# Optimization experiments

Measured on AMD Instinct MI355X. Metric: run time of the kernel, lower is better.

## Reference

```python
import jax, jax.numpy as jnp
import numpy as np

NB_FEATURES = 128
ACCUMULATION = 4


def iterative_inv(mat, n_iter=6):
    # Newton-Schulz iteration for matrix inverse ('original' init: global max)
    I = jnp.eye(mat.shape[-1], dtype=mat.dtype)
    K = mat
    V = (1.0 / jnp.max(jnp.sum(K, axis=-2))) * jnp.swapaxes(K, -1, -2)
    for _ in range(n_iter):
        KV = K @ V
        V = 0.25 * V @ (13.0 * I - KV @ (15.0 * I - KV @ (7.0 * I - KV)))
    return V


def setup_inputs() -> dict:
    key = jax.random.key(0)
    kq, kk, kv, ks = jax.random.split(key, 4)
    b, h, n, d = 4, 8, 2048, 64
    q = jax.random.normal(kq, (b, h, n, d), dtype=jnp.float32)
    k = jax.random.normal(kk, (b, h, n, d), dtype=jnp.float32)
    v = jax.random.normal(kv, (b, h, n, d), dtype=jnp.float32)
    mask = jnp.ones((b, n), dtype=jnp.float32)
    total = ACCUMULATION * NB_FEATURES
    # uniform_sketching: indices in [0,n) scaled by non_padding_num (=n here),
    # second half of the flat index list offset by +n to index the k-block of X.
    S = jax.random.randint(ks, (b, total), 0, n)
    S = S.at[:, total // 2:].add(n)
    sketching_matrix = S.reshape(b, ACCUMULATION, NB_FEATURES)
    random_sign = jnp.ones((b, ACCUMULATION, NB_FEATURES), dtype=jnp.float32)
    return {"q": q, "k": k, "v": v, "mask": mask,
            "random_sign": random_sign, "sketching_matrix": sketching_matrix}


def reference(q, k, v, mask, random_sign, sketching_matrix):
    b, h, n, d = q.shape
    data_normalizer = 32.0 ** (-0.25)
    m = mask[:, None, :, None]                      # [b,1,n,1]
    q = q * (m * data_normalizer)
    k = k * (m * data_normalizer)
    v = v * m

    X = jnp.concatenate([q, k], axis=2)             # [b,h,2n,d]
    Xt = jnp.transpose(X, (0, 2, 1, 3))             # [b,2n,h,d]
    XS = Xt[jnp.arange(b)[:, None, None], sketching_matrix]  # [b,acc,f,h,d]
    XS = jnp.transpose(XS, (0, 3, 1, 2, 4))         # [b,h,acc,f,d]

    # RS-RBF kernel sketch: exp(x.y - |x|^2/2 - |y|^2/2), accumulated over acc
    diag1 = (0.5 * jnp.sum(X * X, axis=-1))[:, :, None, :, None]   # [b,h,1,2n,1]
    diag2 = (0.5 * jnp.sum(XS * XS, axis=-1))[:, :, :, None, :]    # [b,h,acc,1,f]
    prod = jnp.einsum('bhnp,bhmfp->bhmnf', X, XS) - diag1 - diag2  # [b,h,acc,2n,f]
    res = jnp.exp(prod)
    res = jnp.transpose(res, (0, 1, 3, 2, 4))       # [b,h,2n,acc,f]
    AS = jnp.einsum('bhnmf,bmf->bhnf', res, random_sign)  # [b,h,2n,f]

    Q = AS[:, :, :n]                                # [b,h,n,f]
    K = AS[:, :, n:]                                # [b,h,n,f]

    ASt = jnp.transpose(AS, (0, 2, 1, 3))           # [b,2n,h,f]
    STAS = ASt[jnp.arange(b)[:, None, None], sketching_matrix]     # [b,acc,f,h,f]
    STAS = jnp.einsum('bmdhe,bmd->bhde', STAS, random_sign)        # [b,h,f,f]
    f = STAS.shape[-1]
    STAS = STAS + 0.1 * jnp.eye(f, dtype=STAS.dtype)

    D_inv = jnp.sqrt(1.0 / jnp.sum(STAS, axis=-1))  # [b,h,f]
    STAS_n = D_inv[..., :, None] * STAS * D_inv[..., None, :]
    STAS_inv = iterative_inv(STAS_n, 6)

    K = (K * D_inv[:, :, None, :]) @ STAS_inv       # [b,h,n,f]
    K = K * D_inv[:, :, None, :] * m

    context = jnp.einsum('bhnf,bhne->bhfe', K, v)   # [b,h,f,d]
    out = Q @ context                               # [b,h,n,d]
    return out
```

## Files before the change

kernel.cpp:

```cpp
#include <hip/hip_runtime.h>

constexpr int Bc = 4, Hc = 8, Nc = 2048, Dc = 64, Fc = 128, Mc = 4;
constexpr int BHc = Bc*Hc;
constexpr int T2c = 2*Nc;
constexpr int Jc  = Mc*Fc;
constexpr float DNORM = 0.4204482076268573f;

constexpr size_t OFF_AS    = 0;
constexpr size_t OFF_XSH   = OFF_AS    + (size_t)BHc*T2c*Fc;
constexpr size_t OFF_XSM   = OFF_XSH   + (size_t)BHc*Jc*Dc/2;
constexpr size_t OFF_XSL   = OFF_XSM   + (size_t)BHc*Jc*Dc/2;
constexpr size_t OFF_DIAG1 = OFF_XSL   + (size_t)BHc*Jc*Dc/2;
constexpr size_t OFF_DIAG2 = OFF_DIAG1 + (size_t)BHc*T2c;
constexpr size_t OFF_STASN = OFF_DIAG2 + (size_t)BHc*Jc;
constexpr size_t OFF_VBUF  = OFF_STASN + (size_t)BHc*Fc*Fc;
constexpr size_t OFF_DINV  = OFF_VBUF  + (size_t)BHc*Fc*Fc;
constexpr size_t OFF_GMAX  = OFF_DINV  + (size_t)BHc*Fc;
constexpr size_t OFF_CTX   = OFF_GMAX  + 64;
constexpr size_t OFF_KH    = OFF_CTX   + (size_t)BHc*Fc*Dc;
constexpr size_t OFF_KM    = OFF_KH    + (size_t)BHc*Fc*Fc/2;
constexpr size_t OFF_KL    = OFF_KM    + (size_t)BHc*Fc*Fc/2;
constexpr size_t OFF_GPART = OFF_XSH;
constexpr size_t OFF_ZSC   = OFF_GPART + (size_t)BHc*4*128*64;

typedef __attribute__((ext_vector_type(8))) short bf16x8;
typedef __attribute__((ext_vector_type(4))) float f32x4;
typedef __attribute__((ext_vector_type(4))) unsigned short u16x4;

__device__ __forceinline__ unsigned short f2bf_rne(float x) {
  unsigned int u = __float_as_uint(x);
  u += 0x7fff + ((u >> 16) & 1);
  return (unsigned short)(u >> 16);
}
__device__ __forceinline__ float bf2f(unsigned short h) {
  return __uint_as_float(((unsigned int)h) << 16);
}

__global__ __launch_bounds__(256) void diag1_kernel(
    const float* __restrict__ q, const float* __restrict__ k,
    const float* __restrict__ mask, float* __restrict__ diag1) {
  int gid = blockIdx.x*256 + threadIdx.x;
  int kq  = gid & 15;
  int row = gid >> 4;
  int t   = row & (T2c - 1);
  int bh  = row >> 12;
  int b   = bh >> 3;
  int tn  = (t < Nc) ? t : t - Nc;
  const float* src = ((t < Nc) ? q : k) + ((size_t)bh*Nc + tn)*Dc;
  float sc = DNORM * mask[b*Nc + tn];
  float4 x = *(const float4*)(src + kq*4);
  float s = x.x*x.x + x.y*x.y + x.z*x.z + x.w*x.w;
  s += __shfl_xor(s, 1);
  s += __shfl_xor(s, 2);
  s += __shfl_xor(s, 4);
  s += __shfl_xor(s, 8);
  if (kq == 0) diag1[row] = 0.5f * sc * sc * s;
}

__global__ __launch_bounds__(256) void gather_kernel(
    const float* __restrict__ q, const float* __restrict__ k,
    const float* __restrict__ mask, const int* __restrict__ sketch,
    const float* __restrict__ diag1,
    unsigned short* __restrict__ xsh, unsigned short* __restrict__ xsm,
    unsigned short* __restrict__ xsl, float* __restrict__ diag2) {
  int gid = blockIdx.x*256 + threadIdx.x;
  int kq  = gid & 15;
  int idx = gid >> 4;
  int j   = idx & (Jc - 1);
  int bh  = idx >> 9;
  int b   = bh >> 3;
  int t   = sketch[b*Jc + j];
  int tn  = (t < Nc) ? t : t - Nc;
  const float* src = ((t < Nc) ? q : k) + ((size_t)bh*Nc + tn)*Dc;
  float sc = DNORM * mask[b*Nc + tn];
  float4 x = *(const float4*)(src + kq*4);
  float xv[4] = {x.x*sc, x.y*sc, x.z*sc, x.w*sc};
  u16x4 hh, mm_, ll;
  #pragma unroll
  for (int jj = 0; jj < 4; ++jj) {
    unsigned short h = f2bf_rne(xv[jj]);
    float r1 = xv[jj] - bf2f(h);
    unsigned short m = f2bf_rne(r1);
    float r2 = r1 - bf2f(m);
    hh[jj] = h; mm_[jj] = m; ll[jj] = f2bf_rne(r2);
  }
  *(u16x4*)(xsh + (size_t)idx*Dc + kq*4) = hh;
  *(u16x4*)(xsm + (size_t)idx*Dc + kq*4) = mm_;
  *(u16x4*)(xsl + (size_t)idx*Dc + kq*4) = ll;
  if (kq == 0) diag2[idx] = diag1[bh*T2c + t];
}

__device__ __forceinline__ unsigned poff(int r, int ke) {
  unsigned byte = ((unsigned)r << 7) | ((unsigned)ke << 1);
  return byte ^ (((unsigned)(r & 7)) << 4);
}

__global__ __launch_bounds__(512) void as_mfma_kernel(
    const float* __restrict__ q, const float* __restrict__ k,
    const float* __restrict__ mask,
    const unsigned short* __restrict__ xsh, const unsigned short* __restrict__ xsm,
    const unsigned short* __restrict__ xsl,
    const float* __restrict__ diag1, const float* __restrict__ diag2,
    const float* __restrict__ sign, float* __restrict__ AS) {
  extern __shared__ char sma[];
  char* Ah = sma;
  char* Am = sma + 16384;
  char* Al = sma + 32768;
  char* Bh = sma + 49152;
  char* Bm = sma + 65536;
  char* Bl = sma + 81920;
  float* d1s = (float*)(sma + 98304);
  float* d2s = (float*)(sma + 98816);
  float* sgs = (float*)(sma + 100864);
  int bh = blockIdx.y, b = bh >> 3;
  int t0 = blockIdx.x * 128;
  int tid = threadIdx.x;
  int lane = tid & 63, wid = tid >> 6;
  int wr = wid >> 1, wc = wid & 1;
  int l16 = lane & 15, lg = lane >> 4;
  int R0 = wr*32, C0 = wc*64;

  for (int i = tid; i < 128*16; i += 512) {
    int r = i >> 4, kq = i & 15;
    int t = t0 + r;
    int tn = (t < Nc) ? t : t - Nc;
    const float* src = ((t < Nc) ? q : k) + ((size_t)bh*Nc + tn)*Dc + kq*4;
    float sc = DNORM * mask[b*Nc + tn];
    float4 x = *(const float4*)src;
    float xv[4] = {x.x*sc, x.y*sc, x.z*sc, x.w*sc};
    u16x4 hv, mv, lv;
    #pragma unroll
    for (int jj = 0; jj < 4; ++jj) {
      unsigned short h = f2bf_rne(xv[jj]);
      float r1 = xv[jj] - bf2f(h);
      unsigned short m = f2bf_rne(r1);
      float r2 = r1 - bf2f(m);
      hv[jj] = h; mv[jj] = m; lv[jj] = f2bf_rne(r2);
    }
    unsigned off = poff(r, kq*4);
    *(u16x4*)(Ah + off) = hv;
    *(u16x4*)(Am + off) = mv;
    *(u16x4*)(Al + off) = lv;
  }
  if (tid < 128) d1s[tid] = diag1[bh*T2c + t0 + tid];
  for (int i = tid; i < 512; i += 512) {
    d2s[i] = diag2[bh*Jc + i];
    sgs[i] = sign[b*Jc + i];
  }

  const unsigned short* xhh = xsh + (size_t)bh*Jc*Dc;
  const unsigned short* xmm = xsm + (size_t)bh*Jc*Dc;
  const unsigned short* xll = xsl + (size_t)bh*Jc*Dc;
  f32x4 oa[2][4];
  #pragma unroll
  for (int m = 0; m < 2; ++m)
    #pragma unroll
    for (int n = 0; n < 4; ++n) oa[m][n] = 0.f;

  for (int m = 0; m < Mc; ++m) {
    __syncthreads();
    for (int i = tid; i < 128*16; i += 512) {
      int c = i >> 4, k4 = i & 15;
      size_t p = (size_t)(m*Fc + c)*Dc + k4*4;
      unsigned off = poff(c, k4*4);
      *(u16x4*)(Bh + off) = *(const u16x4*)(xhh + p);
      *(u16x4*)(Bm + off) = *(const u16x4*)(xmm + p);
      *(u16x4*)(Bl + off) = *(const u16x4*)(xll + p);
    }
    __syncthreads();

    f32x4 acc[2][4];
    #pragma unroll
    for (int mm = 0; mm < 2; ++mm)
      #pragma unroll
      for (int nn = 0; nn < 4; ++nn) acc[mm][nn] = 0.f;
    #pragma unroll
    for (int kc = 0; kc < Dc; kc += 32) {
      int ko = kc + lg*8;
      bf16x8 ah[2], am2[2], al2[2], bhv[4], bmv[4], blv[4];
      #pragma unroll
      for (int mm = 0; mm < 2; ++mm) {
        unsigned off = poff(R0+16*mm+l16, ko);
        ah[mm]  = *(const bf16x8*)(Ah + off);
        am2[mm] = *(const bf16x8*)(Am + off);
        al2[mm] = *(const bf16x8*)(Al + off);
      }
      #pragma unroll
      for (int nn = 0; nn < 4; ++nn) {
        unsigned off = poff(C0+16*nn+l16, ko);
        bhv[nn] = *(const bf16x8*)(Bh + off);
        bmv[nn] = *(const bf16x8*)(Bm + off);
        blv[nn] = *(const bf16x8*)(Bl + off);
      }
      #pragma unroll
      for (int mm = 0; mm < 2; ++mm)
        #pragma unroll
        for (int nn = 0; nn < 4; ++nn) {
          acc[mm][nn] = __builtin_amdgcn_mfma_f32_16x16x32_bf16(am2[mm], bmv[nn], acc[mm][nn], 0,0,0);
          acc[mm][nn] = __builtin_amdgcn_mfma_f32_16x16x32_bf16(ah[mm],  blv[nn], acc[mm][nn], 0,0,0);
          acc[mm][nn] = __builtin_amdgcn_mfma_f32_16x16x32_bf16(al2[mm], bhv[nn], acc[mm][nn], 0,0,0);
          acc[mm][nn] = __builtin_amdgcn_mfma_f32_16x16x32_bf16(ah[mm],  bmv[nn], acc[mm][nn], 0,0,0);
          acc[mm][nn] = __builtin_amdgcn_mfma_f32_16x16x32_bf16(am2[mm], bhv[nn], acc[mm][nn], 0,0,0);
          acc[mm][nn] = __builtin_amdgcn_mfma_f32_16x16x32_bf16(ah[mm],  bhv[nn], acc[mm][nn], 0,0,0);
        }
    }
    #pragma unroll
    for (int mm = 0; mm < 2; ++mm)
      #pragma unroll
      for (int nn = 0; nn < 4; ++nn) {
        int c = C0 + 16*nn + l16;
        float d2v = d2s[m*Fc + c], sg = sgs[m*Fc + c];
        #pragma unroll
        for (int r = 0; r < 4; ++r) {
          int row = R0 + 16*mm + 4*lg + r;
          oa[mm][nn][r] += sg * __expf(acc[mm][nn][r] - d1s[row] - d2v);
        }
      }
  }
  #pragma unroll
  for (int mm = 0; mm < 2; ++mm)
    #pragma unroll
    for (int nn = 0; nn < 4; ++nn) {
      int c = C0 + 16*nn + l16;
      #pragma unroll
      for (int r = 0; r < 4; ++r) {
        int row = R0 + 16*mm + 4*lg + r;
        AS[((size_t)bh*T2c + t0 + row)*Fc + c] = oa[mm][nn][r];
      }
    }
}

__global__ __launch_bounds__(256) void stas_kernel(
    const float* __restrict__ AS, const int* __restrict__ sketch,
    const float* __restrict__ sign,
    float* __restrict__ STASn, float* __restrict__ Dinv,
    unsigned short* __restrict__ Kh, unsigned short* __restrict__ Km,
    unsigned short* __restrict__ Kl,
    unsigned int* __restrict__ gmax) {
  extern __shared__ float stas[];
  __shared__ int   Ssh[Jc];
  __shared__ float sgn[Jc];
  __shared__ float Dl[Fc];
  __shared__ float red[Fc];
  int bh = blockIdx.x;
  int b  = bh >> 3;
  int tid = threadIdx.x;
  for (int i = tid; i < Jc; i += 256) {
    Ssh[i] = sketch[b*Jc + i];
    sgn[i] = sign[b*Jc + i];
  }
  __syncthreads();
  for (int i = tid; i < Fc*Fc; i += 256) {
    int dd = i >> 7, e = i & 127;
    float vsum = 0.f;
    #pragma unroll
    for (int m = 0; m < Mc; ++m) {
      int t = Ssh[m*Fc + dd];
      vsum += sgn[m*Fc + dd] * AS[((size_t)bh*T2c + t)*Fc + e];
    }
    if (dd == e) vsum += 0.1f;
    stas[dd*129 + e] = vsum;
  }
  __syncthreads();
  if (tid < Fc) {
    float s = 0.f;
    for (int e = 0; e < Fc; ++e) s += stas[tid*129 + e];
    float di = 1.0f / sqrtf(s);
    Dl[tid] = di;
    Dinv[bh*Fc + tid] = di;
  }
  __syncthreads();
  for (int i = tid; i < Fc*Fc; i += 256) {
    int dd = i >> 7, e = i & 127;
    float vv = stas[dd*129 + e] * Dl[dd] * Dl[e];
    stas[dd*129 + e] = vv;
    STASn[(size_t)bh*Fc*Fc + i] = vv;
    unsigned short hb = f2bf_rne(vv); float r1 = vv - bf2f(hb);
    unsigned short mb = f2bf_rne(r1); float r2 = r1 - bf2f(mb);
    Kh[(size_t)bh*Fc*Fc + i] = hb;
    Km[(size_t)bh*Fc*Fc + i] = mb;
    Kl[(size_t)bh*Fc*Fc + i] = f2bf_rne(r2);
  }
  __syncthreads();
  if (tid < Fc) {
    float s = 0.f;
    for (int dd = 0; dd < Fc; ++dd) s += stas[dd*129 + tid];
    red[tid] = s;
  }
  __syncthreads();
  if (tid == 0) {
    float mx = 0.f;
    for (int e = 0; e < Fc; ++e) mx = fmaxf(mx, red[e]);
    atomicMax(gmax, __float_as_uint(mx));
  }
}

__device__ __forceinline__ unsigned boff(int brow, int ke) {
  unsigned byte = ((unsigned)brow << 8) | ((unsigned)ke << 1);
  return byte ^ (((unsigned)(brow & 7)) << 4);
}

__device__ __forceinline__ void mm6(const bf16x8 ah[2], const bf16x8 am[2], const bf16x8 al[2],
                                    const bf16x8 bh[4], const bf16x8 bm[4], const bf16x8 bl[4],
                                    f32x4 acc[2][4]) {
  #pragma unroll
  for (int m = 0; m < 2; ++m)
    #pragma unroll
    for (int n = 0; n < 4; ++n) {
      acc[m][n] = __builtin_amdgcn_mfma_f32_16x16x32_bf16(am[m], bm[n], acc[m][n], 0,0,0);
      acc[m][n] = __builtin_amdgcn_mfma_f32_16x16x32_bf16(ah[m], bl[n], acc[m][n], 0,0,0);
      acc[m][n] = __builtin_amdgcn_mfma_f32_16x16x32_bf16(al[m], bh[n], acc[m][n], 0,0,0);
      acc[m][n] = __builtin_amdgcn_mfma_f32_16x16x32_bf16(ah[m], bm[n], acc[m][n], 0,0,0);
      acc[m][n] = __builtin_amdgcn_mfma_f32_16x16x32_bf16(am[m], bh[n], acc[m][n], 0,0,0);
      acc[m][n] = __builtin_amdgcn_mfma_f32_16x16x32_bf16(ah[m], bh[n], acc[m][n], 0,0,0);
    }
}

__device__ __forceinline__ void ld3(const char* Ph, const char* Pm, const char* Pl,
                                    int brow, int ko, bf16x8& h, bf16x8& m, bf16x8& l) {
  unsigned off = boff(brow, ko);
  h = *(const bf16x8*)(Ph + off);
  m = *(const bf16x8*)(Pm + off);
  l = *(const bf16x8*)(Pl + off);
}

__device__ __forceinline__ void mm_p1(
    const unsigned short* __restrict__ kh, const unsigned short* __restrict__ km,
    const unsigned short* __restrict__ kl,
    const char* Ah, const char* Am, const char* Al,
    int R0, int C0, int l16, int lg, f32x4 acc[2][4]) {
  #pragma unroll 2
  for (int kc = 0; kc < Fc; kc += 32) {
    int ko = kc + lg*8;
    bf16x8 ah[2], am[2], al[2], bh[4], bm[4], bl[4];
    #pragma unroll
    for (int m = 0; m < 2; ++m) {
      size_t p = (size_t)(R0+16*m+l16)*Fc + ko;
      ah[m] = *(const bf16x8*)(kh + p);
      am[m] = *(const bf16x8*)(km + p);
      al[m] = *(const bf16x8*)(kl + p);
    }
    #pragma unroll
    for (int n = 0; n < 4; ++n)
      ld3(Ah, Am, Al, C0+16*n+l16, ko, bh[n], bm[n], bl[n]);
    mm6(ah, am, al, bh, bm, bl, acc);
  }
}

__device__ __forceinline__ void mm_p234(
    const char* Ah, const char* Am, const char* Al,
    const char* Zh, const char* Zm, const unsigned short* __restrict__ ZlG,
    int R0, int C0, int l16, int lg, f32x4 acc[2][4]) {
  #pragma unroll 1
  for (int kc = 0; kc < Fc; kc += 32) {
    int ko = kc + lg*8;
    bf16x8 ah[2], am[2], al[2], bh[4], bm[4], bl[4];
    #pragma unroll
    for (int m = 0; m < 2; ++m)
      ld3(Ah, Am, Al, R0+16*m+l16, ko, ah[m], am[m], al[m]);
    #pragma unroll
    for (int n = 0; n < 4; ++n) {
      int col = C0+16*n+l16;
      unsigned off = boff(col, ko);
      bh[n] = *(const bf16x8*)(Zh + off);
      bm[n] = *(const bf16x8*)(Zm + off);
      bl[n] = *(const bf16x8*)(ZlG + col*Fc + ko);
    }
    mm6(ah, am, al, bh, bm, bl, acc);
  }
}

__device__ __forceinline__ void split4(f32x4 v, u16x4& hv, u16x4& mv, u16x4& lv) {
  #pragma unroll
  for (int r = 0; r < 4; ++r) {
    unsigned short hb = f2bf_rne(v[r]); float r1 = v[r] - bf2f(hb);
    unsigned short mb = f2bf_rne(r1);   float r2 = r1 - bf2f(mb);
    hv[r] = hb; mv[r] = mb; lv[r] = f2bf_rne(r2);
  }
}
__device__ __forceinline__ void wbA3(char* Ah, char* Am, char* Al,
                                     int col, int row0, f32x4 v) {
  u16x4 hv, mv, lv;
  split4(v, hv, mv, lv);
  unsigned off = boff(col, row0);
  *(u16x4*)(Ah + off) = hv;
  *(u16x4*)(Am + off) = mv;
  *(u16x4*)(Al + off) = lv;
}
__device__ __forceinline__ void wbZ3(char* Zh, char* Zm, unsigned short* __restrict__ ZlG,
                                     int col, int row0, f32x4 v) {
  u16x4 hv, mv, lv;
  split4(v, hv, mv, lv);
  unsigned off = boff(col, row0);
  *(u16x4*)(Zh + off) = hv;
  *(u16x4*)(Zm + off) = mv;
  *(u16x4*)(ZlG + col*Fc + row0) = lv;
}

__global__ __launch_bounds__(512) void newton_ctx_kernel(
    const float* __restrict__ STASn,
    const unsigned short* __restrict__ KhG, const unsigned short* __restrict__ KmG,
    const unsigned short* __restrict__ KlG,
    const float* __restrict__ gmaxf, float* __restrict__ Vout,
    const float* __restrict__ ASg, const float* __restrict__ vg,
    const float* __restrict__ maskg, float* __restrict__ Gpart,
    unsigned short* __restrict__ ZlScr) {
  extern __shared__ char smc[];
  int tid  = threadIdx.x;

  if (blockIdx.x < BHc) {
    char* Ah = smc;
    char* Am = smc + 32768;
    char* Al = smc + 65536;
    char* Zh = smc + 98304;
    char* Zm = smc + 131072;
    int bh = blockIdx.x;
    const float* Kp = STASn + (size_t)bh*Fc*Fc;
    const unsigned short* kh = KhG + (size_t)bh*Fc*Fc;
    const unsigned short* km = KmG + (size_t)bh*Fc*Fc;
    const unsigned short* kl = KlG + (size_t)bh*Fc*Fc;
    unsigned short* ZlG = ZlScr + (size_t)bh*Fc*Fc;
    float ginv = 1.0f / gmaxf[0];
    int lane = tid & 63;
    int wid  = tid >> 6;
    int wr = wid >> 1, wc = wid & 1;
    int l16 = lane & 15, lg = lane >> 4;
    int R0 = wr*32, C0 = wc*64;
    int drow0 = lg*4;

    f32x4 vreg[2][4];
    #pragma unroll
    for (int m = 0; m < 2; ++m)
      #pragma unroll
      for (int n = 0; n < 4; ++n) {
        int col = C0 + 16*n + l16;
        #pragma unroll
        for (int r = 0; r < 4; ++r)
          vreg[m][n][r] = Kp[(size_t)(R0 + 16*m + drow0 + r)*Fc + col] * ginv;
        wbA3(Ah, Am, Al, col, R0 + 16*m + drow0, vreg[m][n]);
      }
    __syncthreads();

    f32x4 fin[2][4];
    for (int it = 0; it < 6; ++it) {
      f32x4 acc[2][4];
      #pragma unroll
      for (int m = 0; m < 2; ++m) for (int n = 0; n < 4; ++n) acc[m][n] = 0.f;
      mm_p1(kh, km, kl, Ah, Am, Al, R0, C0, l16, lg, acc);
      #pragma unroll
      for (int m = 0; m < 2; ++m)
        #pragma unroll
        for (int n = 0; n < 4; ++n)
          wbZ3(Zh, Zm, ZlG, C0 + 16*n + l16, R0 + 16*m + drow0, acc[m][n]);
      __syncthreads();

      #pragma unroll
      for (int m = 0; m < 2; ++m) for (int n = 0; n < 4; ++n) acc[m][n] = 0.f;
      mm_p234(Ah, Am, Al, Zh, Zm, ZlG, R0, C0, l16, lg, acc);
      #pragma unroll
      for (int m = 0; m < 2; ++m)
        #pragma unroll
        for (int n = 0; n < 4; ++n)
          fin[m][n] = 13.f*vreg[m][n] - 15.f*acc[m][n];
      __syncthreads();
      #pragma unroll
      for (int m = 0; m < 2; ++m)
        #pragma unroll
        for (int n = 0; n < 4; ++n)
          wbA3(Ah, Am, Al, C0 + 16*n + l16, R0 + 16*m + drow0, acc[m][n]);
      __syncthreads();

      #pragma unroll
      for (int m = 0; m < 2; ++m) for (int n = 0; n < 4; ++n) acc[m][n] = 0.f;
      mm_p234(Ah, Am, Al, Zh, Zm, ZlG, R0, C0, l16, lg, acc);
      #pragma unroll
      for (int m = 0; m < 2; ++m)
        #pragma unroll
        for (int n = 0; n < 4; ++n)
          fin[m][n] += 7.f*acc[m][n];
      __syncthreads();
      #pragma unroll
      for (int m = 0; m < 2; ++m)
        #pragma unroll
        for (int n = 0; n < 4; ++n)
          wbA3(Ah, Am, Al, C0 + 16*n + l16, R0 + 16*m + drow0, acc[m][n]);
      __syncthreads();

      #pragma unroll
      for (int m = 0; m < 2; ++m) for (int n = 0; n < 4; ++n) acc[m][n] = 0.f;
      mm_p234(Ah, Am, Al, Zh, Zm, ZlG, R0, C0, l16, lg, acc);
      #pragma unroll
      for (int m = 0; m < 2; ++m)
        #pragma unroll
        for (int n = 0; n < 4; ++n) {
          fin[m][n] = 0.25f*(fin[m][n] - acc[m][n]);
          vreg[m][n] = fin[m][n];
        }
      __syncthreads();
      #pragma unroll
      for (int m = 0; m < 2; ++m)
        #pragma unroll
        for (int n = 0; n < 4; ++n)
          wbA3(Ah, Am, Al, C0 + 16*n + l16, R0 + 16*m + drow0, fin[m][n]);
      __syncthreads();
    }

    float* Vo = Vout + (size_t)bh*Fc*Fc;
    #pragma unroll
    for (int m = 0; m < 2; ++m)
      #pragma unroll
      for (int n = 0; n < 4; ++n) {
        int col = C0 + 16*n + l16;
        #pragma unroll
        for (int r = 0; r < 4; ++r)
          Vo[(size_t)(R0 + 16*m + drow0 + r)*Fc + col] = vreg[m][n][r];
      }
  } else {
    float* Ksh = (float*)smc;
    float* vsh = (float*)(smc + 32768);
    int id = blockIdx.x - BHc;
    int cbh = id >> 2, chunk = id & 3;
    int cb = cbh >> 3;
    int t0 = chunk * 512;
    int f = tid & 127, g = tid >> 7;
    float acc[16];
    #pragma unroll
    for (int j = 0; j < 16; ++j) acc[j] = 0.f;
    for (int sub = 0; sub < 8; ++sub) {
      __syncthreads();
      int ts = t0 + sub*64;
      for (int i = tid; i < 64*32; i += 512) {
        int r = i >> 5, c4 = i & 31;
        *(float4*)&Ksh[r*128 + c4*4] =
            *(const float4*)(ASg + ((size_t)cbh*T2c + Nc + ts + r)*Fc + c4*4);
      }
      for (int i = tid; i < 64*16; i += 512) {
        int r = i >> 4, c4 = i & 15;
        float mk = maskg[cb*Nc + ts + r];
        float m2 = mk*mk;
        float4 x = *(const float4*)(vg + ((size_t)cbh*Nc + ts + r)*Dc + c4*4);
        x.x*=m2; x.y*=m2; x.z*=m2; x.w*=m2;
        *(float4*)&vsh[r*64 + c4*4] = x;
      }
      __syncthreads();
      #pragma unroll 2
      for (int tl = 0; tl < 64; ++tl) {
        float kf = Ksh[tl*128 + f];
        #pragma unroll
        for (int j4 = 0; j4 < 4; ++j4) {
          float4 vv = *(const float4*)&vsh[tl*64 + g*16 + j4*4];
          acc[j4*4+0] += kf*vv.x; acc[j4*4+1] += kf*vv.y;
          acc[j4*4+2] += kf*vv.z; acc[j4*4+3] += kf*vv.w;
        }
      }
    }
    float* gp = Gpart + ((((size_t)cbh*4 + chunk)*128 + f)*64 + g*16);
    #pragma unroll
    for (int j4 = 0; j4 < 4; ++j4)
      *(float4*)(gp + j4*4) = *(const float4*)&acc[j4*4];
  }
}

__global__ __launch_bounds__(256) void ctx_fix_kernel(
    const float* __restrict__ Gpart, const float* __restrict__ Vinv,
    const float* __restrict__ Dinv, float* __restrict__ ctxo) {
  __shared__ float DG[128*64];
  __shared__ float Dl[128];
  int bh = blockIdx.x;
  int tid = threadIdx.x;
  if (tid < 128) Dl[tid] = Dinv[bh*Fc + tid];
  __syncthreads();
  for (int i = tid; i < 2048; i += 256) {
    int e = i >> 4, c4 = i & 15;
    const float* g0 = Gpart + ((((size_t)bh*4)*128 + e)*64 + c4*4);
    float4 s0 = *(const float4*)(g0);
    float4 s1 = *(const float4*)(g0 + 8192);
    float4 s2 = *(const float4*)(g0 + 16384);
    float4 s3 = *(const float4*)(g0 + 24576);
    float de = Dl[e];
    float4 o;
    o.x = (s0.x+s1.x+s2.x+s3.x)*de;
    o.y = (s0.y+s1.y+s2.y+s3.y)*de;
    o.z = (s0.z+s1.z+s2.z+s3.z)*de;
    o.w = (s0.w+s1.w+s2.w+s3.w)*de;
    *(float4*)&DG[e*64 + c4*4] = o;
  }
  __syncthreads();
  int f = tid & 127, half = tid >> 7;
  float acc[32];
  #pragma unroll
  for (int j = 0; j < 32; ++j) acc[j] = 0.f;
  for (int e = 0; e < 128; ++e) {
    float s = Vinv[(size_t)bh*Fc*Fc + (size_t)e*Fc + f];
    #pragma unroll
    for (int j4 = 0; j4 < 8; ++j4) {
      float4 dg = *(const float4*)&DG[e*64 + half*32 + j4*4];
      acc[j4*4+0] += s*dg.x; acc[j4*4+1] += s*dg.y;
      acc[j4*4+2] += s*dg.z; acc[j4*4+3] += s*dg.w;
    }
  }
  float df = Dl[f];
  float* op = ctxo + (size_t)bh*Fc*Dc + f*Dc + half*32;
  #pragma unroll
  for (int j4 = 0; j4 < 8; ++j4) {
    float4 o;
    o.x = acc[j4*4+0]*df; o.y = acc[j4*4+1]*df;
    o.z = acc[j4*4+2]*df; o.w = acc[j4*4+3]*df;
    *(float4*)(op + j4*4) = o;
  }
}

__global__ __launch_bounds__(256) void out_kernel(
    const float* __restrict__ AS, const float* __restrict__ ctx,
    float* __restrict__ out) {
  extern __shared__ float smo[];
  float* Asq = smo;
  float* Cs  = smo + 64*132;
  int bh = blockIdx.y;
  int row0 = blockIdx.x * 64;
  int tid = threadIdx.x;
  int tr = tid >> 4, tc = tid & 15;
  for (int i = tid; i < 64*32; i += 256) {
    int r = i >> 5, kq = i & 31;
    *(float4*)&Asq[r*132 + kq*4] =
        *(const float4*)(AS + ((size_t)bh*T2c + row0 + r)*Fc + kq*4);
  }
  for (int i = tid; i < 128*16; i += 256) {
    int r = i >> 4, kq = i & 15;
    *(float4*)&Cs[r*64 + kq*4] =
        *(const float4*)(ctx + (size_t)bh*Fc*Dc + r*Dc + kq*4);
  }
  __syncthreads();
  float acc[4][4] = {};
  #pragma unroll 2
  for (int kk = 0; kk < Fc; ++kk) {
    float4 bv = *(const float4*)&Cs[kk*64 + tc*4];
    float a0 = Asq[(tr*4+0)*132 + kk];
    float a1 = Asq[(tr*4+1)*132 + kk];
    float a2 = Asq[(tr*4+2)*132 + kk];
    float a3 = Asq[(tr*4+3)*132 + kk];
    acc[0][0] += a0*bv.x; acc[0][1] += a0*bv.y; acc[0][2] += a0*bv.z; acc[0][3] += a0*bv.w;
    acc[1][0] += a1*bv.x; acc[1][1] += a1*bv.y; acc[1][2] += a1*bv.z; acc[1][3] += a1*bv.w;
    acc[2][0] += a2*bv.x; acc[2][1] += a2*bv.y; acc[2][2] += a2*bv.z; acc[2][3] += a2*bv.w;
    acc[3][0] += a3*bv.x; acc[3][1] += a3*bv.y; acc[3][2] += a3*bv.z; acc[3][3] += a3*bv.w;
  }
  #pragma unroll
  for (int i = 0; i < 4; ++i) {
    float4 o;
    o.x = acc[i][0]; o.y = acc[i][1]; o.z = acc[i][2]; o.w = acc[i][3];
    *(float4*)(out + ((size_t)bh*Nc + row0 + tr*4 + i)*Dc + tc*4) = o;
  }
}

extern "C" void kernel_launch(void* const* d_in, const int* in_sizes, int n_in,
                              void* d_out, int out_size, void* d_ws, size_t ws_size,
                              hipStream_t stream) {
  const float* q    = (const float*)d_in[0];
  const float* k    = (const float*)d_in[1];
  const float* v    = (const float*)d_in[2];
  const float* mask = (const float*)d_in[3];
  const float* sign = (const float*)d_in[4];
  const int*   sketch = (const int*)d_in[5];
  float* out = (float*)d_out;
  float* ws  = (float*)d_ws;

  unsigned short* xsh = (unsigned short*)(ws + OFF_XSH);
  unsigned short* xsm = (unsigned short*)(ws + OFF_XSM);
  unsigned short* xsl = (unsigned short*)(ws + OFF_XSL);
  unsigned short* kh  = (unsigned short*)(ws + OFF_KH);
  unsigned short* km  = (unsigned short*)(ws + OFF_KM);
  unsigned short* kl  = (unsigned short*)(ws + OFF_KL);
  unsigned short* zsc = (unsigned short*)(ws + OFF_ZSC);

  hipMemsetAsync(ws + OFF_GMAX, 0, sizeof(float), stream);

  diag1_kernel<<<BHc*T2c*16/256, 256, 0, stream>>>(q, k, mask, ws + OFF_DIAG1);
  gather_kernel<<<BHc*Jc*16/256, 256, 0, stream>>>(q, k, mask, sketch, ws + OFF_DIAG1,
                                                   xsh, xsm, xsl, ws + OFF_DIAG2);
  as_mfma_kernel<<<dim3(T2c/128, BHc), 512, 102912, stream>>>(q, k, mask, xsh, xsm, xsl,
      ws + OFF_DIAG1, ws + OFF_DIAG2, sign, ws + OFF_AS);
  stas_kernel<<<BHc, 256, 128*129*sizeof(float), stream>>>(ws + OFF_AS, sketch, sign,
      ws + OFF_STASN, ws + OFF_DINV, kh, km, kl, (unsigned int*)(ws + OFF_GMAX));
  newton_ctx_kernel<<<BHc + 128, 512, 163840, stream>>>(ws + OFF_STASN, kh, km, kl,
      ws + OFF_GMAX, ws + OFF_VBUF, ws + OFF_AS, v, mask, ws + OFF_GPART, zsc);
  ctx_fix_kernel<<<BHc, 256, 0, stream>>>(ws + OFF_GPART, ws + OFF_VBUF,
      ws + OFF_DINV, ws + OFF_CTX);
  out_kernel<<<dim3(Nc/64, BHc), 256, (64*132 + 128*64)*sizeof(float), stream>>>(
      ws + OFF_AS, ws + OFF_CTX, out);
}
```

Baseline: 331.6 us.

## Compute sketched AS rows first and overlap full AS with Newton iterations

A new small kernel computes the RBF sketch only for the 512 sketched rows per head. STAS is now built from those rows, so it no longer has to wait for the full AS matrix. The full AS computation moves into the same launch as the serial Newton-Schulz inverse, running on the spare blocks while the 32 Newton blocks work. The context accumulation becomes its own kernel afterwards. In exchange, the sketched rows' exponentials are computed twice (about one eighth extra AS work) and the launch gains an extra kernel. The scratch buffer is moved so it no longer aliases the gather buffers, which are now still being read during the Newton launch.

After: 343.3 us. +3.5%, slower.

```diff
diff --git a/kernel.cpp b/kernel.cpp
--- a/kernel.cpp
+++ b/kernel.cpp
@@ -20,8 +20,9 @@
 constexpr size_t OFF_KH    = OFF_CTX   + (size_t)BHc*Fc*Dc;
 constexpr size_t OFF_KM    = OFF_KH    + (size_t)BHc*Fc*Fc/2;
 constexpr size_t OFF_KL    = OFF_KM    + (size_t)BHc*Fc*Fc/2;
+constexpr size_t OFF_ZSC   = OFF_KL    + (size_t)BHc*Fc*Fc/2;
 constexpr size_t OFF_GPART = OFF_XSH;
-constexpr size_t OFF_ZSC   = OFF_GPART + (size_t)BHc*4*128*64;
+constexpr size_t OFF_ASS   = OFF_AS;
 
 typedef __attribute__((ext_vector_type(8))) short bf16x8;
 typedef __attribute__((ext_vector_type(4))) float f32x4;
@@ -95,14 +96,10 @@
   return byte ^ (((unsigned)(r & 7)) << 4);
 }
 
-__global__ __launch_bounds__(512) void as_mfma_kernel(
-    const float* __restrict__ q, const float* __restrict__ k,
-    const float* __restrict__ mask,
-    const unsigned short* __restrict__ xsh, const unsigned short* __restrict__ xsm,
-    const unsigned short* __restrict__ xsl,
-    const float* __restrict__ diag1, const float* __restrict__ diag2,
-    const float* __restrict__ sign, float* __restrict__ AS) {
-  extern __shared__ char sma[];
+__device__ __forceinline__ void as_body(
+    char* sma, const unsigned short* xhh, const unsigned short* xmm,
+    const unsigned short* xll, float* __restrict__ dst, size_t dst_row_stride_base,
+    int tid) {
   char* Ah = sma;
   char* Am = sma + 16384;
   char* Al = sma + 32768;
@@ -112,45 +109,11 @@
   float* d1s = (float*)(sma + 98304);
   float* d2s = (float*)(sma + 98816);
   float* sgs = (float*)(sma + 100864);
-  int bh = blockIdx.y, b = bh >> 3;
-  int t0 = blockIdx.x * 128;
-  int tid = threadIdx.x;
   int lane = tid & 63, wid = tid >> 6;
   int wr = wid >> 1, wc = wid & 1;
   int l16 = lane & 15, lg = lane >> 4;
   int R0 = wr*32, C0 = wc*64;
 
-  for (int i = tid; i < 128*16; i += 512) {
-    int r = i >> 4, kq = i & 15;
-    int t = t0 + r;
-    int tn = (t < Nc) ? t : t - Nc;
-    const float* src = ((t < Nc) ? q : k) + ((size_t)bh*Nc + tn)*Dc + kq*4;
-    float sc = DNORM * mask[b*Nc + tn];
-    float4 x = *(const float4*)src;
-    float xv[4] = {x.x*sc, x.y*sc, x.z*sc, x.w*sc};
-    u16x4 hv, mv, lv;
-    #pragma unroll
-    for (int jj = 0; jj < 4; ++jj) {
-      unsigned short h = f2bf_rne(xv[jj]);
-      float r1 = xv[jj] - bf2f(h);
-      unsigned short m = f2bf_rne(r1);
-      float r2 = r1 - bf2f(m);
-      hv[jj] = h; mv[jj] = m; lv[jj] = f2bf_rne(r2);
-    }
-    unsigned off = poff(r, kq*4);
-    *(u16x4*)(Ah + off) = hv;
-    *(u16x4*)(Am + off) = mv;
-    *(u16x4*)(Al + off) = lv;
-  }
-  if (tid < 128) d1s[tid] = diag1[bh*T2c + t0 + tid];
-  for (int i = tid; i < 512; i += 512) {
-    d2s[i] = diag2[bh*Jc + i];
-    sgs[i] = sign[b*Jc + i];
-  }
-
-  const unsigned short* xhh = xsh + (size_t)bh*Jc*Dc;
-  const unsigned short* xmm = xsm + (size_t)bh*Jc*Dc;
-  const unsigned short* xll = xsl + (size_t)bh*Jc*Dc;
   f32x4 oa[2][4];
   #pragma unroll
   for (int m = 0; m < 2; ++m)
@@ -225,39 +188,64 @@
       #pragma unroll
       for (int r = 0; r < 4; ++r) {
         int row = R0 + 16*mm + 4*lg + r;
-        AS[((size_t)bh*T2c + t0 + row)*Fc + c] = oa[mm][nn][r];
+        dst[dst_row_stride_base + (size_t)row*Fc + c] = oa[mm][nn][r];
       }
     }
 }
 
+__global__ __launch_bounds__(512) void ass_mfma_kernel(
+    const unsigned short* __restrict__ xsh, const unsigned short* __restrict__ xsm,
+    const unsigned short* __restrict__ xsl,
+    const float* __restrict__ diag2, const float* __restrict__ sign,
+    float* __restrict__ ASS) {
+  extern __shared__ char sma[];
+  float* d1s = (float*)(sma + 98304);
+  float* d2s = (float*)(sma + 98816);
+  float* sgs = (float*)(sma + 100864);
+  int bh = blockIdx.y, b = bh >> 3;
+  int j0 = blockIdx.x * 128;
+  int tid = threadIdx.x;
+  const unsigned short* xhh = xsh + (size_t)bh*Jc*Dc;
+  const unsigned short* xmm = xsm + (size_t)bh*Jc*Dc;
+  const unsigned short* xll = xsl + (size_t)bh*Jc*Dc;
+
+  for (int i = tid; i < 128*16; i += 512) {
+    int r = i >> 4, kq = i & 15;
+    size_t p = (size_t)(j0 + r)*Dc + kq*4;
+    unsigned off = poff(r, kq*4);
+    *(u16x4*)(sma + off)         = *(const u16x4*)(xhh + p);
+    *(u16x4*)(sma + 16384 + off) = *(const u16x4*)(xmm + p);
+    *(u16x4*)(sma + 32768 + off) = *(const u16x4*)(xll + p);
+  }
+  if (tid < 128) d1s[tid] = diag2[bh*Jc + j0 + tid];
+  for (int i = tid; i < 512; i += 512) {
+    d2s[i] = diag2[bh*Jc + i];
+    sgs[i] = sign[b*Jc + i];
+  }
+  as_body(sma, xhh, xmm, xll, ASS, (size_t)bh*Jc*Fc + (size_t)j0*Fc, tid);
+}
+
 __global__ __launch_bounds__(256) void stas_kernel(
-    const float* __restrict__ AS, const int* __restrict__ sketch,
-    const float* __restrict__ sign,
+    const float* __restrict__ ASS, const float* __restrict__ sign,
     float* __restrict__ STASn, float* __restrict__ Dinv,
     unsigned short* __restrict__ Kh, unsigned short* __restrict__ Km,
     unsigned short* __restrict__ Kl,
     unsigned int* __restrict__ gmax) {
   extern __shared__ float stas[];
-  __shared__ int   Ssh[Jc];
   __shared__ float sgn[Jc];
   __shared__ float Dl[Fc];
   __shared__ float red[Fc];
   int bh = blockIdx.x;
   int b  = bh >> 3;
   int tid = threadIdx.x;
-  for (int i = tid; i < Jc; i += 256) {
-    Ssh[i] = sketch[b*Jc + i];
-    sgn[i] = sign[b*Jc + i];
-  }
+  for (int i = tid; i < Jc; i += 256) sgn[i] = sign[b*Jc + i];
   __syncthreads();
   for (int i = tid; i < Fc*Fc; i += 256) {
     int dd = i >> 7, e = i & 127;
     float vsum = 0.f;
     #pragma unroll
-    for (int m = 0; m < Mc; ++m) {
-      int t = Ssh[m*Fc + dd];
-      vsum += sgn[m*Fc + dd] * AS[((size_t)bh*T2c + t)*Fc + e];
-    }
+    for (int m = 0; m < Mc; ++m)
+      vsum += sgn[m*Fc + dd] * ASS[((size_t)bh*Jc + m*Fc + dd)*Fc + e];
     if (dd == e) vsum += 0.1f;
     stas[dd*129 + e] = vsum;
   }
@@ -397,14 +385,18 @@
   *(u16x4*)(ZlG + col*Fc + row0) = lv;
 }
 
-__global__ __launch_bounds__(512) void newton_ctx_kernel(
+__global__ __launch_bounds__(512) void newton_as_kernel(
     const float* __restrict__ STASn,
     const unsigned short* __restrict__ KhG, const unsigned short* __restrict__ KmG,
     const unsigned short* __restrict__ KlG,
     const float* __restrict__ gmaxf, float* __restrict__ Vout,
-    const float* __restrict__ ASg, const float* __restrict__ vg,
-    const float* __restrict__ maskg, float* __restrict__ Gpart,
-    unsigned short* __restrict__ ZlScr) {
+    unsigned short* __restrict__ ZlScr,
+    const float* __restrict__ q, const float* __restrict__ k,
+    const float* __restrict__ mask,
+    const unsigned short* __restrict__ xsh, const unsigned short* __restrict__ xsm,
+    const unsigned short* __restrict__ xsl,
+    const float* __restrict__ diag1, const float* __restrict__ diag2,
+    const float* __restrict__ sign, float* __restrict__ AS) {
   extern __shared__ char smc[];
   int tid  = threadIdx.x;
 
@@ -516,49 +508,94 @@
           Vo[(size_t)(R0 + 16*m + drow0 + r)*Fc + col] = vreg[m][n][r];
       }
   } else {
-    float* Ksh = (float*)smc;
-    float* vsh = (float*)(smc + 32768);
     int id = blockIdx.x - BHc;
-    int cbh = id >> 2, chunk = id & 3;
-    int cb = cbh >> 3;
-    int t0 = chunk * 512;
-    int f = tid & 127, g = tid >> 7;
-    float acc[16];
-    #pragma unroll
-    for (int j = 0; j < 16; ++j) acc[j] = 0.f;
-    for (int sub = 0; sub < 8; ++sub) {
-      __syncthreads();
-      int ts = t0 + sub*64;
-      for (int i = tid; i < 64*32; i += 512) {
-        int r = i >> 5, c4 = i & 31;
-        *(float4*)&Ksh[r*128 + c4*4] =
-            *(const float4*)(ASg + ((size_t)cbh*T2c + Nc + ts + r)*Fc + c4*4);
+    int bh = id >> 5, b = bh >> 3;
+    int t0 = (id & 31) * 128;
+    float* d1s = (float*)(smc + 98304);
+    float* d2s = (float*)(smc + 98816);
+    float* sgs = (float*)(smc + 100864);
+
+    for (int i = tid; i < 128*16; i += 512) {
+      int r = i >> 4, kq = i & 15;
+      int t = t0 + r;
+      int tn = (t < Nc) ? t : t - Nc;
+      const float* src = ((t < Nc) ? q : k) + ((size_t)bh*Nc + tn)*Dc + kq*4;
+      float sc = DNORM * mask[b*Nc + tn];
+      float4 x = *(const float4*)src;
+      float xv[4] = {x.x*sc, x.y*sc, x.z*sc, x.w*sc};
+      u16x4 hv, mv, lv;
+      #pragma unroll
+      for (int jj = 0; jj < 4; ++jj) {
+        unsigned short h = f2bf_rne(xv[jj]);
+        float r1 = xv[jj] - bf2f(h);
+        unsigned short m = f2bf_rne(r1);
+        float r2 = r1 - bf2f(m);
+        hv[jj] = h; mv[jj] = m; lv[jj] = f2bf_rne(r2);
       }
-      for (int i = tid; i < 64*16; i += 512) {
-        int r = i >> 4, c4 = i & 15;
-        float mk = maskg[cb*Nc + ts + r];
-        float m2 = mk*mk;
-        float4 x = *(const float4*)(vg + ((size_t)cbh*Nc + ts + r)*Dc + c4*4);
-        x.x*=m2; x.y*=m2; x.z*=m2; x.w*=m2;
-        *(float4*)&vsh[r*64 + c4*4] = x;
+      unsigned off = poff(r, kq*4);
+      *(u16x4*)(smc + off)         = hv;
+      *(u16x4*)(smc + 16384 + off) = mv;
+      *(u16x4*)(smc + 32768 + off) = lv;
+    }
+    if (tid < 128) d1s[tid] = diag1[bh*T2c + t0 + tid];
+    for (int i = tid; i < 512; i += 512) {
+      d2s[i] = diag2[bh*Jc + i];
+      sgs[i] = sign[b*Jc + i];
+    }
+    const unsigned short* xhh = xsh + (size_t)bh*Jc*Dc;
+    const unsigned short* xmm = xsm + (size_t)bh*Jc*Dc;
+    const unsigned short* xll = xsl + (size_t)bh*Jc*Dc;
+    as_body(smc, xhh, xmm, xll, AS, (size_t)bh*T2c*Fc + (size_t)t0*Fc, tid);
+  }
+}
+
+__global__ __launch_bounds__(512) void ctx_raw_kernel(
+    const float* __restrict__ ASg, const float* __restrict__ vg,
+    const float* __restrict__ maskg, float* __restrict__ Gpart) {
+  extern __shared__ char smc[];
+  float* Ksh = (float*)smc;
+  float* vsh = (float*)(smc + 32768);
+  int id = blockIdx.x;
+  int cbh = id >> 2, chunk = id & 3;
+  int cb = cbh >> 3;
+  int t0 = chunk * 512;
+  int tid = threadIdx.x;
+  int f = tid & 127, g = tid >> 7;
+  float acc[16];
+  #pragma unroll
+  for (int j = 0; j < 16; ++j) acc[j] = 0.f;
+  for (int sub = 0; sub < 8; ++sub) {
+    __syncthreads();
+    int ts = t0 + sub*64;
+    for (int i = tid; i < 64*32; i += 512) {
+      int r = i >> 5, c4 = i & 31;
+      *(float4*)&Ksh[r*128 + c4*4] =
+          *(const float4*)(ASg + ((size_t)cbh*T2c + Nc + ts + r)*Fc + c4*4);
+    }
+    for (int i = tid; i < 64*16; i += 512) {
+      int r = i >> 4, c4 = i & 15;
+      float mk = maskg[cb*Nc + ts + r];
+      float m2 = mk*mk;
+      float4 x = *(const float4*)(vg + ((size_t)cbh*Nc + ts + r)*Dc + c4*4);
+      x.x*=m2; x.y*=m2; x.z*=m2; x.w*=m2;
+      *(float4*)&vsh[r*64 + c4*4] = x;
+    }
+    __syncthreads();
+    #pragma unroll 2
+    for (int tl = 0; tl < 64; ++tl) {
+      float kf = Ksh[tl*128 + f];
+      #pragma unroll
+      for (int j4 = 0; j4 < 4; ++j4) {
+        float4 vv = *(const float4*)&vsh[tl*64 + g*16 + j4*4];
+        acc[j4*4+0] += kf*vv.x; acc[j4*4+1] += kf*vv.y;
+        acc[j4*4+2] += kf*vv.z; acc[j4*4+3] += kf*vv.w;
       }
-      __syncthreads();
-      #pragma unroll 2
-      for (int tl = 0; tl < 64; ++tl) {
-        float kf = Ksh[tl*128 + f];
-        #pragma unroll
-        for (int j4 = 0; j4 < 4; ++j4) {
-          float4 vv = *(const float4*)&vsh[tl*64 + g*16 + j4*4];
-          acc[j4*4+0] += kf*vv.x; acc[j4*4+1] += kf*vv.y;
-          acc[j4*4+2] += kf*vv.z; acc[j4*4+3] += kf*vv.w;
-        }
-      }
-    }
-    float* gp = Gpart + ((((size_t)cbh*4 + chunk)*128 + f)*64 + g*16);
-    #pragma unroll
-    for (int j4 = 0; j4 < 4; ++j4)
-      *(float4*)(gp + j4*4) = *(const float4*)&acc[j4*4];
-  }
+    }
+  }
+  float* gp = Gpart + ((((size_t)cbh*4 + chunk)*128 + f)*64 + g*16);
+  #pragma unroll
+  for (int j4 = 0; j4 < 4; ++j4)
+    *(float4*)(gp + j4*4) = *(const float4*)&acc[j4*4];
 }
 
 __global__ __launch_bounds__(256) void ctx_fix_kernel(
@@ -677,12 +714,14 @@
   diag1_kernel<<<BHc*T2c*16/256, 256, 0, stream>>>(q, k, mask, ws + OFF_DIAG1);
   gather_kernel<<<BHc*Jc*16/256, 256, 0, stream>>>(q, k, mask, sketch, ws + OFF_DIAG1,
                                                    xsh, xsm, xsl, ws + OFF_DIAG2);
-  as_mfma_kernel<<<dim3(T2c/128, BHc), 512, 102912, stream>>>(q, k, mask, xsh, xsm, xsl,
-      ws + OFF_DIAG1, ws + OFF_DIAG2, sign, ws + OFF_AS);
-  stas_kernel<<<BHc, 256, 128*129*sizeof(float), stream>>>(ws + OFF_AS, sketch, sign,
+  ass_mfma_kernel<<<dim3(Jc/128, BHc), 512, 102912, stream>>>(xsh, xsm, xsl,
+      ws + OFF_DIAG2, sign, ws + OFF_ASS);
+  stas_kernel<<<BHc, 256, 128*129*sizeof(float), stream>>>(ws + OFF_ASS, sign,
       ws + OFF_STASN, ws + OFF_DINV, kh, km, kl, (unsigned int*)(ws + OFF_GMAX));
-  newton_ctx_kernel<<<BHc + 128, 512, 163840, stream>>>(ws + OFF_STASN, kh, km, kl,
-      ws + OFF_GMAX, ws + OFF_VBUF, ws + OFF_AS, v, mask, ws + OFF_GPART, zsc);
+  newton_as_kernel<<<BHc + BHc*(T2c/128), 512, 163840, stream>>>(
+      ws + OFF_STASN, kh, km, kl, ws + OFF_GMAX, ws + OFF_VBUF, zsc,
+      q, k, mask, xsh, xsm, xsl, ws + OFF_DIAG1, ws + OFF_DIAG2, sign, ws + OFF_AS);
+  ctx_raw_kernel<<<128, 512, 49152, stream>>>(ws + OFF_AS, v, mask, ws + OFF_GPART);
   ctx_fix_kernel<<<BHc, 256, 0, stream>>>(ws + OFF_GPART, ws + OFF_VBUF,
       ws + OFF_DINV, ws + OFF_CTX);
   out_kernel<<<dim3(Nc/64, BHc), 256, (64*132 + 128*64)*sizeof(float), stream>>>(
```
